# Kernel tuning notes

Hardware: AMD Instinct MI355X
Metric: run time of the kernel (lower is better)

## Reference

```python
import jax, jax.numpy as jnp
import numpy as np

DIM = 1024
NHEADS = 16
DIM_HEAD = 64
HIDDEN = NHEADS * DIM_HEAD  # 1024


def _xavier(key, fan_in, fan_out):
    limit = np.sqrt(6.0 / (fan_in + fan_out))
    return jax.random.uniform(key, (fan_in, fan_out), jnp.float32, -limit, limit)


def setup_inputs() -> dict:
    key = jax.random.key(0)
    kq, k1, k2, k3 = jax.random.split(key, 4)
    q = jax.random.normal(kq, (2, 2048, DIM), jnp.float32)
    Wq = _xavier(k1, DIM, HIDDEN)
    bq = jnp.zeros((HIDDEN,), jnp.float32)
    Wkv = _xavier(k2, DIM, 2 * HIDDEN)
    bkv = jnp.zeros((2 * HIDDEN,), jnp.float32)
    Wo = _xavier(k3, HIDDEN, DIM)
    bo = jnp.zeros((DIM,), jnp.float32)
    return {"q": q, "Wq": Wq, "bq": bq, "Wkv": Wkv, "bkv": bkv, "Wo": Wo, "bo": bo}


def reference(q, Wq, bq, Wkv, bkv, Wo, bo):
    scale = DIM_HEAD ** (-0.5)
    query = q @ Wq + bq                      # [b, s, hidden]
    kv = q @ Wkv + bkv                       # self-attention: kv from q
    key_, value = jnp.split(kv, 2, axis=-1)  # [b, s, hidden] each
    b, s, _ = query.shape
    query = query.reshape(b, s, NHEADS, DIM_HEAD)
    key_ = key_.reshape(b, s, NHEADS, DIM_HEAD)
    value = value.reshape(b, s, NHEADS, DIM_HEAD)
    scores = jnp.einsum('bqhd,bkhd->bhqk', query, key_) * scale
    attn = jax.nn.softmax(scores, axis=-1)
    out = jnp.einsum('bhqk,bkhd->bqhd', attn, value)
    out = out.reshape(b, s, HIDDEN)
    return out @ Wo + bo
```

## Files before the change

kernel.cpp:

```cpp
#include <hip/hip_runtime.h>

#define DIM 1024
#define NHEADS 16
#define DH 64
#define BATCH 2
#define SEQ 2048

typedef float f32x4 __attribute__((ext_vector_type(4)));
typedef short s16x8 __attribute__((ext_vector_type(8)));

__device__ __forceinline__ short f2bf(float f) {
    union { float f; unsigned u; } v; v.f = f;
    unsigned r = v.u + 0x7fffu + ((v.u >> 16) & 1u);
    return (short)(r >> 16);
}

__device__ __forceinline__ void gld16(const void* g, void* l) {
    __builtin_amdgcn_global_load_lds(
        (const __attribute__((address_space(1))) void*)g,
        (__attribute__((address_space(3))) void*)l, 16, 0, 0);
}

__global__ __launch_bounds__(256) void convert_bf16_kernel(
    const float* __restrict__ X, short* __restrict__ Y)
{
    const int i = (blockIdx.x * 256 + threadIdx.x) * 8;
    float4 a = *(const float4*)(X + i);
    float4 b = *(const float4*)(X + i + 4);
    s16x8 o;
    o[0] = f2bf(a.x); o[1] = f2bf(a.y); o[2] = f2bf(a.z); o[3] = f2bf(a.w);
    o[4] = f2bf(b.x); o[5] = f2bf(b.y); o[6] = f2bf(b.z); o[7] = f2bf(b.w);
    *(s16x8*)(Y + i) = o;
}

__global__ __launch_bounds__(256) void transpose_bf16_kernel(
    const float* __restrict__ W, short* __restrict__ WT, int N)
{
    const int t  = threadIdx.x;
    const int n  = blockIdx.x * 64 + (t & 63);
    const int k0 = (blockIdx.y * 4 + (t >> 6)) * 8;
    s16x8 o;
#pragma unroll
    for (int j = 0; j < 8; ++j) o[j] = f2bf(W[(size_t)(k0 + j) * N + n]);
    *(s16x8*)&WT[(size_t)n * 1024 + k0] = o;
}

template<int TM, bool OUT_BF16>
__global__ __launch_bounds__(256) void gemm_mfma_kernel(
    const short* __restrict__ A, const short* __restrict__ Bt,
    const float* __restrict__ bias, void* __restrict__ C, int M, int N)
{
    const int K = 1024;
    constexpr int NI = (TM == 128) ? 4 : 2;
    __shared__ short As[TM * 32];
    __shared__ short Bs[128 * 32];

    const int t    = threadIdx.x;
    const int wave = t >> 6;
    const int lane = t & 63;
    const int col  = lane & 15;
    const int quad = lane >> 4;
    const int m0 = blockIdx.y * TM;
    const int n0 = blockIdx.x * 128;
    const int wroff = (TM == 128) ? (wave >> 1) * 64 : 0;
    const int wcoff = (TM == 128) ? (wave & 1) * 64 : wave * 32;

    f32x4 acc[4][NI];
#pragma unroll
    for (int mi = 0; mi < 4; ++mi)
#pragma unroll
        for (int ni = 0; ni < NI; ++ni) acc[mi][ni] = (f32x4){0.f, 0.f, 0.f, 0.f};

    constexpr int RPW = TM / 4;
    const int ldrowA = wave * RPW + (lane >> 2);
    const int ldrowB = wave * 32  + (lane >> 2);
    const int ldcol  = (lane & 3) * 8;
    const short* Ag = A  + (size_t)(m0 + ldrowA) * K + ldcol;
    const short* Bg = Bt + (size_t)(n0 + ldrowB) * K + ldcol;
    short* AsW = &As[wave * RPW * 32];
    short* BsW = &Bs[wave * 1024];

    for (int k0 = 0; k0 < K; k0 += 32) {
        __syncthreads();
        gld16(Ag + k0, AsW);
        if (TM == 128) gld16(Ag + 16 * K + k0, AsW + 512);
        gld16(Bg + k0,          BsW);
        gld16(Bg + 16 * K + k0, BsW + 512);
        __syncthreads();

        s16x8 aA[4], bB[NI];
#pragma unroll
        for (int mi = 0; mi < 4; ++mi)
            aA[mi] = *(const s16x8*)&As[(wroff + 16 * mi + col) * 32 + quad * 8];
#pragma unroll
        for (int ni = 0; ni < NI; ++ni)
            bB[ni] = *(const s16x8*)&Bs[(wcoff + 16 * ni + col) * 32 + quad * 8];
#pragma unroll
        for (int mi = 0; mi < 4; ++mi)
#pragma unroll
            for (int ni = 0; ni < NI; ++ni)
                acc[mi][ni] = __builtin_amdgcn_mfma_f32_16x16x32_bf16(aA[mi], bB[ni], acc[mi][ni], 0, 0, 0);
    }

    float bias_v[NI];
#pragma unroll
    for (int ni = 0; ni < NI; ++ni) bias_v[ni] = bias[n0 + wcoff + 16 * ni + col];

#pragma unroll
    for (int mi = 0; mi < 4; ++mi)
#pragma unroll
        for (int ni = 0; ni < NI; ++ni)
#pragma unroll
            for (int r = 0; r < 4; ++r) {
                const int gm = m0 + wroff + 16 * mi + quad * 4 + r;
                const int gn = n0 + wcoff + 16 * ni + col;
                float v = acc[mi][ni][r] + bias_v[ni];
                if (OUT_BF16) ((short*)C)[(size_t)gm * N + gn] = f2bf(v);
                else          ((float*)C)[(size_t)gm * N + gn] = v;
            }
}

__global__ __launch_bounds__(256) void attn_mfma_kernel(
    const short* __restrict__ Q,
    const short* __restrict__ KV,
    short* __restrict__ O)
{
    const int qt = blockIdx.x;
    const int h  = blockIdx.y;
    const int b  = blockIdx.z;
    const int t  = threadIdx.x;
    const int wave = t >> 6;
    const int lane = t & 63;
    const int col  = lane & 15;
    const int quad = lane >> 4;

    __shared__ short Ps[128 * 72];
    __shared__ short Ks[64 * 72];
    __shared__ short Vt[64 * 72];

    const short* Qg = Q  + ((size_t)(b * SEQ + qt * 128)) * DIM + h * DH;
    const short* Kg = KV + (size_t)b * SEQ * (2 * DIM) + h * DH;
    const short* Vg = Kg + DIM;
    short*       Og = O  + ((size_t)(b * SEQ + qt * 128)) * DIM + h * DH;

    const int L_r = t >> 3;
    const int L_c = (t & 7) * 8;

#pragma unroll
    for (int p = 0; p < 4; ++p) {
        int rr = p * 32 + L_r;
        *(s16x8*)&Ps[rr * 72 + L_c] = *(const s16x8*)(Qg + (size_t)rr * DIM + L_c);
    }
    __syncthreads();

    const int qb = wave * 32;
    s16x8 aQ[2][2];
#pragma unroll
    for (int mi = 0; mi < 2; ++mi)
#pragma unroll
        for (int kq = 0; kq < 2; ++kq)
            aQ[mi][kq] = *(const s16x8*)&Ps[(qb + 16 * mi + col) * 72 + kq * 32 + quad * 8];

    f32x4 oa[2][4];
    float lsum[2][4];
#pragma unroll
    for (int mi = 0; mi < 2; ++mi) {
#pragma unroll
        for (int tt = 0; tt < 4; ++tt) oa[mi][tt] = (f32x4){0.f, 0.f, 0.f, 0.f};
#pragma unroll
        for (int r = 0; r < 4; ++r) lsum[mi][r] = 0.f;
    }

    s16x8 kx[2], vx[2];
#pragma unroll
    for (int p = 0; p < 2; ++p) {
        size_t go = (size_t)(p * 32 + L_r) * (2 * DIM) + L_c;
        kx[p] = *(const s16x8*)(Kg + go);
        vx[p] = *(const s16x8*)(Vg + go);
    }

    for (int kt = 0; kt < SEQ / 64; ++kt) {
        __syncthreads();
#pragma unroll
        for (int p = 0; p < 2; ++p) {
            int rr = p * 32 + L_r;
            *(s16x8*)&Ks[rr * 72 + L_c] = kx[p];
#pragma unroll
            for (int jj = 0; jj < 8; ++jj) {
                int dv = L_c + jj;
                Vt[dv * 72 + (rr & 7) + 8 * (((rr >> 3) ^ (dv >> 3)) & 7)] = vx[p][jj];
            }
        }
        {
            int nt = (kt + 1 < SEQ / 64) ? kt + 1 : kt;
            const short* Kt = Kg + (size_t)(nt * 64) * (2 * DIM);
            const short* Vv = Vg + (size_t)(nt * 64) * (2 * DIM);
#pragma unroll
            for (int p = 0; p < 2; ++p) {
                size_t go = (size_t)(p * 32 + L_r) * (2 * DIM) + L_c;
                kx[p] = *(const s16x8*)(Kt + go);
                vx[p] = *(const s16x8*)(Vv + go);
            }
        }
        __syncthreads();

        s16x8 bK[4][2];
#pragma unroll
        for (int tt = 0; tt < 4; ++tt)
#pragma unroll
            for (int kq = 0; kq < 2; ++kq)
                bK[tt][kq] = *(const s16x8*)&Ks[(16 * tt + col) * 72 + kq * 32 + quad * 8];
        f32x4 sc[2][4];
#pragma unroll
        for (int mi = 0; mi < 2; ++mi)
#pragma unroll
            for (int tt = 0; tt < 4; ++tt) {
                f32x4 a = (f32x4){0.f, 0.f, 0.f, 0.f};
                a = __builtin_amdgcn_mfma_f32_16x16x32_bf16(aQ[mi][0], bK[tt][0], a, 0, 0, 0);
                a = __builtin_amdgcn_mfma_f32_16x16x32_bf16(aQ[mi][1], bK[tt][1], a, 0, 0, 0);
                sc[mi][tt] = a;
            }

#pragma unroll
        for (int mi = 0; mi < 2; ++mi)
#pragma unroll
            for (int tt = 0; tt < 4; ++tt)
#pragma unroll
                for (int r = 0; r < 4; ++r) {
                    float p = __expf(sc[mi][tt][r] * 0.125f);
                    lsum[mi][r] += p;
                    Ps[(qb + 16 * mi + quad * 4 + r) * 72 + 16 * tt + col] = f2bf(p);
                }

        asm volatile("s_waitcnt lgkmcnt(0)" ::: "memory");

        s16x8 aP[2][2];
#pragma unroll
        for (int mi = 0; mi < 2; ++mi)
#pragma unroll
            for (int ks = 0; ks < 2; ++ks)
                aP[mi][ks] = *(const s16x8*)&Ps[(qb + 16 * mi + col) * 72 + ks * 32 + quad * 8];
#pragma unroll
        for (int tt = 0; tt < 4; ++tt) {
            const int dv = 16 * tt + col;
            s16x8 bv0 = *(const s16x8*)&Vt[dv * 72 + 8 * ((quad     ^ (dv >> 3)) & 7)];
            s16x8 bv1 = *(const s16x8*)&Vt[dv * 72 + 8 * (((4 + quad) ^ (dv >> 3)) & 7)];
#pragma unroll
            for (int mi = 0; mi < 2; ++mi) {
                oa[mi][tt] = __builtin_amdgcn_mfma_f32_16x16x32_bf16(aP[mi][0], bv0, oa[mi][tt], 0, 0, 0);
                oa[mi][tt] = __builtin_amdgcn_mfma_f32_16x16x32_bf16(aP[mi][1], bv1, oa[mi][tt], 0, 0, 0);
            }
        }
    }

    float inv[2][4];
#pragma unroll
    for (int mi = 0; mi < 2; ++mi)
#pragma unroll
        for (int r = 0; r < 4; ++r) {
            float s = lsum[mi][r];
            s += __shfl_xor(s, 1);
            s += __shfl_xor(s, 2);
            s += __shfl_xor(s, 4);
            s += __shfl_xor(s, 8);
            inv[mi][r] = 1.f / s;
        }
#pragma unroll
    for (int mi = 0; mi < 2; ++mi)
#pragma unroll
        for (int tt = 0; tt < 4; ++tt)
#pragma unroll
            for (int r = 0; r < 4; ++r)
                Og[(size_t)(qb + 16 * mi + quad * 4 + r) * DIM + 16 * tt + col] =
                    f2bf(oa[mi][tt][r] * inv[mi][r]);
}

extern "C" void kernel_launch(void* const* d_in, const int* in_sizes, int n_in,
                              void* d_out, int out_size, void* d_ws, size_t ws_size,
                              hipStream_t stream)
{
    const float* q   = (const float*)d_in[0];
    const float* Wq  = (const float*)d_in[1];
    const float* bq  = (const float*)d_in[2];
    const float* Wkv = (const float*)d_in[3];
    const float* bkv = (const float*)d_in[4];
    const float* Wo  = (const float*)d_in[5];
    const float* bo  = (const float*)d_in[6];
    float* out = (float*)d_out;

    const int M = BATCH * SEQ;

    short* qb    = (short*)d_ws;
    short* WqT   = qb    + (size_t)M * DIM;
    short* WkvT  = WqT   + (size_t)DIM * DIM;
    short* WoT   = WkvT  + (size_t)DIM * 2 * DIM;
    short* Qbuf  = WoT   + (size_t)DIM * DIM;
    short* KVbuf = Qbuf  + (size_t)M * DIM;
    short* AObuf = KVbuf + (size_t)M * 2 * DIM;

    convert_bf16_kernel<<<(M * DIM) / (256 * 8), 256, 0, stream>>>(q, qb);
    transpose_bf16_kernel<<<dim3(DIM / 64, 32), 256, 0, stream>>>(Wq, WqT, DIM);
    transpose_bf16_kernel<<<dim3(2 * DIM / 64, 32), 256, 0, stream>>>(Wkv, WkvT, 2 * DIM);
    transpose_bf16_kernel<<<dim3(DIM / 64, 32), 256, 0, stream>>>(Wo, WoT, DIM);

    gemm_mfma_kernel<64, true><<<dim3(DIM / 128, M / 64), 256, 0, stream>>>(qb, WqT, bq, Qbuf, M, DIM);
    gemm_mfma_kernel<128, true><<<dim3(2 * DIM / 128, M / 128), 256, 0, stream>>>(qb, WkvT, bkv, KVbuf, M, 2 * DIM);
    attn_mfma_kernel<<<dim3(SEQ / 128, NHEADS, BATCH), 256, 0, stream>>>(Qbuf, KVbuf, AObuf);
    gemm_mfma_kernel<64, false><<<dim3(DIM / 128, M / 64), 256, 0, stream>>>(AObuf, WoT, bo, out, M, DIM);
}
```

Before: 224.7 us.

## Fuse Q and KV projections and rewrite attention with split-K waves

```diff
diff --git a/kernel.cpp b/kernel.cpp
--- a/kernel.cpp
+++ b/kernel.cpp
@@ -8,6 +8,7 @@
 
 typedef float f32x4 __attribute__((ext_vector_type(4)));
 typedef short s16x8 __attribute__((ext_vector_type(8)));
+typedef short s16x4 __attribute__((ext_vector_type(4)));
 
 __device__ __forceinline__ short f2bf(float f) {
     union { float f; unsigned u; } v; v.f = f;
@@ -48,7 +49,8 @@
 template<int TM, bool OUT_BF16>
 __global__ __launch_bounds__(256) void gemm_mfma_kernel(
     const short* __restrict__ A, const short* __restrict__ Bt,
-    const float* __restrict__ bias, void* __restrict__ C, int M, int N)
+    const float* __restrict__ bias0, const float* __restrict__ bias1, int nsplit,
+    void* __restrict__ C, int M, int N)
 {
     const int K = 1024;
     constexpr int NI = (TM == 128) ? 4 : 2;
@@ -104,7 +106,10 @@
 
     float bias_v[NI];
 #pragma unroll
-    for (int ni = 0; ni < NI; ++ni) bias_v[ni] = bias[n0 + wcoff + 16 * ni + col];
+    for (int ni = 0; ni < NI; ++ni) {
+        int nb = n0 + wcoff + 16 * ni + col;
+        bias_v[ni] = (nb < nsplit) ? bias0[nb] : bias1[nb - nsplit];
+    }
 
 #pragma unroll
     for (int mi = 0; mi < 4; ++mi)
@@ -120,9 +125,8 @@
             }
 }
 
-__global__ __launch_bounds__(256) void attn_mfma_kernel(
-    const short* __restrict__ Q,
-    const short* __restrict__ KV,
+__global__ __launch_bounds__(512) void attn_v5_kernel(
+    const short* __restrict__ QKV,
     short* __restrict__ O)
 {
     const int qt = blockIdx.x;
@@ -133,146 +137,158 @@
     const int lane = t & 63;
     const int col  = lane & 15;
     const int quad = lane >> 4;
-
-    __shared__ short Ps[128 * 72];
-    __shared__ short Ks[64 * 72];
-    __shared__ short Vt[64 * 72];
-
-    const short* Qg = Q  + ((size_t)(b * SEQ + qt * 128)) * DIM + h * DH;
-    const short* Kg = KV + (size_t)b * SEQ * (2 * DIM) + h * DH;
-    const short* Vg = Kg + DIM;
-    short*       Og = O  + ((size_t)(b * SEQ + qt * 128)) * DIM + h * DH;
-
-    const int L_r = t >> 3;
-    const int L_c = (t & 7) * 8;
-
-#pragma unroll
-    for (int p = 0; p < 4; ++p) {
-        int rr = p * 32 + L_r;
-        *(s16x8*)&Ps[rr * 72 + L_c] = *(const s16x8*)(Qg + (size_t)rr * DIM + L_c);
-    }
-    __syncthreads();
-
-    const int qb = wave * 32;
-    s16x8 aQ[2][2];
-#pragma unroll
-    for (int mi = 0; mi < 2; ++mi)
+    const int wq = wave & 3;
+    const int kh = wave >> 2;
+
+    __shared__ short Ks[2][64 * 72];
+    __shared__ short Vt[2][64 * 72];
+    __shared__ short Ps[8][64 * 40];
+
+    const short* Qg = QKV + (size_t)(b * SEQ + qt * 256) * 3072 + h * DH;
+    const short* Kg = QKV + (size_t)(b * SEQ) * 3072 + 1024 + h * DH;
+    const short* Vg = Kg + 1024;
+
+    s16x8 aQ[4][2];
+#pragma unroll
+    for (int tq = 0; tq < 4; ++tq)
 #pragma unroll
         for (int kq = 0; kq < 2; ++kq)
-            aQ[mi][kq] = *(const s16x8*)&Ps[(qb + 16 * mi + col) * 72 + kq * 32 + quad * 8];
-
-    f32x4 oa[2][4];
-    float lsum[2][4];
-#pragma unroll
-    for (int mi = 0; mi < 2; ++mi) {
-#pragma unroll
-        for (int tt = 0; tt < 4; ++tt) oa[mi][tt] = (f32x4){0.f, 0.f, 0.f, 0.f};
-#pragma unroll
-        for (int r = 0; r < 4; ++r) lsum[mi][r] = 0.f;
-    }
-
-    s16x8 kx[2], vx[2];
-#pragma unroll
-    for (int p = 0; p < 2; ++p) {
-        size_t go = (size_t)(p * 32 + L_r) * (2 * DIM) + L_c;
-        kx[p] = *(const s16x8*)(Kg + go);
-        vx[p] = *(const s16x8*)(Vg + go);
-    }
+            aQ[tq][kq] = *(const s16x8*)(Qg + (size_t)(wq * 64 + 16 * tq + col) * 3072 + kq * 32 + quad * 8);
+
+    f32x4 oa[4][4];
+    float lsum[4] = {0.f, 0.f, 0.f, 0.f};
+#pragma unroll
+    for (int td = 0; td < 4; ++td)
+#pragma unroll
+        for (int tq = 0; tq < 4; ++tq) oa[td][tq] = (f32x4){0.f, 0.f, 0.f, 0.f};
+
+    const int srow = t >> 3;
+    const int sc8  = (t & 7) * 8;
+    const short* KgS = Kg + (size_t)srow * 3072 + sc8;
+    const short* VgS = Vg + (size_t)srow * 3072 + sc8;
+    s16x8 kx = *(const s16x8*)KgS;
+    s16x8 vx = *(const s16x8*)VgS;
+
+    short* PsW = &Ps[wave][0];
 
     for (int kt = 0; kt < SEQ / 64; ++kt) {
-        __syncthreads();
-#pragma unroll
-        for (int p = 0; p < 2; ++p) {
-            int rr = p * 32 + L_r;
-            *(s16x8*)&Ks[rr * 72 + L_c] = kx[p];
-#pragma unroll
-            for (int jj = 0; jj < 8; ++jj) {
-                int dv = L_c + jj;
-                Vt[dv * 72 + (rr & 7) + 8 * (((rr >> 3) ^ (dv >> 3)) & 7)] = vx[p][jj];
-            }
+        const int cur = kt & 1;
+        *(s16x8*)&Ks[cur][srow * 72 + sc8] = kx;
+#pragma unroll
+        for (int jj = 0; jj < 8; ++jj) {
+            int dv = sc8 + jj;
+            Vt[cur][dv * 72 + (srow & 7) + 8 * (((srow >> 3) ^ (dv >> 3)) & 7)] = vx[jj];
         }
         {
             int nt = (kt + 1 < SEQ / 64) ? kt + 1 : kt;
-            const short* Kt = Kg + (size_t)(nt * 64) * (2 * DIM);
-            const short* Vv = Vg + (size_t)(nt * 64) * (2 * DIM);
-#pragma unroll
-            for (int p = 0; p < 2; ++p) {
-                size_t go = (size_t)(p * 32 + L_r) * (2 * DIM) + L_c;
-                kx[p] = *(const s16x8*)(Kt + go);
-                vx[p] = *(const s16x8*)(Vv + go);
+            kx = *(const s16x8*)(KgS + (size_t)nt * 64 * 3072);
+            vx = *(const s16x8*)(VgS + (size_t)nt * 64 * 3072);
+        }
+        __syncthreads();
+
+        s16x8 aK[2][2];
+#pragma unroll
+        for (int tk = 0; tk < 2; ++tk)
+#pragma unroll
+            for (int kq = 0; kq < 2; ++kq)
+                aK[tk][kq] = *(const s16x8*)&Ks[cur][(kh * 32 + 16 * tk + col) * 72 + kq * 32 + quad * 8];
+        f32x4 st[2][4];
+#pragma unroll
+        for (int tk = 0; tk < 2; ++tk)
+#pragma unroll
+            for (int tq = 0; tq < 4; ++tq) {
+                f32x4 a = (f32x4){0.f, 0.f, 0.f, 0.f};
+                a = __builtin_amdgcn_mfma_f32_16x16x32_bf16(aK[tk][0], aQ[tq][0], a, 0, 0, 0);
+                a = __builtin_amdgcn_mfma_f32_16x16x32_bf16(aK[tk][1], aQ[tq][1], a, 0, 0, 0);
+                st[tk][tq] = a;
             }
-        }
-        __syncthreads();
-
-        s16x8 bK[4][2];
-#pragma unroll
-        for (int tt = 0; tt < 4; ++tt)
-#pragma unroll
-            for (int kq = 0; kq < 2; ++kq)
-                bK[tt][kq] = *(const s16x8*)&Ks[(16 * tt + col) * 72 + kq * 32 + quad * 8];
-        f32x4 sc[2][4];
-#pragma unroll
-        for (int mi = 0; mi < 2; ++mi)
-#pragma unroll
-            for (int tt = 0; tt < 4; ++tt) {
-                f32x4 a = (f32x4){0.f, 0.f, 0.f, 0.f};
-                a = __builtin_amdgcn_mfma_f32_16x16x32_bf16(aQ[mi][0], bK[tt][0], a, 0, 0, 0);
-                a = __builtin_amdgcn_mfma_f32_16x16x32_bf16(aQ[mi][1], bK[tt][1], a, 0, 0, 0);
-                sc[mi][tt] = a;
+
+#pragma unroll
+        for (int tk = 0; tk < 2; ++tk)
+#pragma unroll
+            for (int tq = 0; tq < 4; ++tq) {
+                float p0 = __expf(st[tk][tq][0] * 0.125f);
+                float p1 = __expf(st[tk][tq][1] * 0.125f);
+                float p2 = __expf(st[tk][tq][2] * 0.125f);
+                float p3 = __expf(st[tk][tq][3] * 0.125f);
+                lsum[tq] += (p0 + p1) + (p2 + p3);
+                s16x4 pk;
+                pk[0] = f2bf(p0); pk[1] = f2bf(p1); pk[2] = f2bf(p2); pk[3] = f2bf(p3);
+                *(s16x4*)&PsW[(16 * tq + col) * 40 + 16 * tk + quad * 4] = pk;
             }
-
-#pragma unroll
-        for (int mi = 0; mi < 2; ++mi)
-#pragma unroll
-            for (int tt = 0; tt < 4; ++tt)
-#pragma unroll
-                for (int r = 0; r < 4; ++r) {
-                    float p = __expf(sc[mi][tt][r] * 0.125f);
-                    lsum[mi][r] += p;
-                    Ps[(qb + 16 * mi + quad * 4 + r) * 72 + 16 * tt + col] = f2bf(p);
-                }
-
         asm volatile("s_waitcnt lgkmcnt(0)" ::: "memory");
 
-        s16x8 aP[2][2];
-#pragma unroll
-        for (int mi = 0; mi < 2; ++mi)
-#pragma unroll
-            for (int ks = 0; ks < 2; ++ks)
-                aP[mi][ks] = *(const s16x8*)&Ps[(qb + 16 * mi + col) * 72 + ks * 32 + quad * 8];
-#pragma unroll
-        for (int tt = 0; tt < 4; ++tt) {
-            const int dv = 16 * tt + col;
-            s16x8 bv0 = *(const s16x8*)&Vt[dv * 72 + 8 * ((quad     ^ (dv >> 3)) & 7)];
-            s16x8 bv1 = *(const s16x8*)&Vt[dv * 72 + 8 * (((4 + quad) ^ (dv >> 3)) & 7)];
-#pragma unroll
-            for (int mi = 0; mi < 2; ++mi) {
-                oa[mi][tt] = __builtin_amdgcn_mfma_f32_16x16x32_bf16(aP[mi][0], bv0, oa[mi][tt], 0, 0, 0);
-                oa[mi][tt] = __builtin_amdgcn_mfma_f32_16x16x32_bf16(aP[mi][1], bv1, oa[mi][tt], 0, 0, 0);
+        s16x8 bP[4];
+#pragma unroll
+        for (int tq = 0; tq < 4; ++tq)
+            bP[tq] = *(const s16x8*)&PsW[(16 * tq + col) * 40 + quad * 8];
+#pragma unroll
+        for (int td = 0; td < 4; ++td) {
+            const int dv = 16 * td + col;
+            s16x8 aV = *(const s16x8*)&Vt[cur][dv * 72 + 8 * (((kh * 4 + quad) ^ (dv >> 3)) & 7)];
+#pragma unroll
+            for (int tq = 0; tq < 4; ++tq)
+                oa[td][tq] = __builtin_amdgcn_mfma_f32_16x16x32_bf16(aV, bP[tq], oa[td][tq], 0, 0, 0);
+        }
+    }
+
+#pragma unroll
+    for (int tq = 0; tq < 4; ++tq) {
+        lsum[tq] += __shfl_xor(lsum[tq], 16);
+        lsum[tq] += __shfl_xor(lsum[tq], 32);
+    }
+
+    __syncthreads();
+    float* red  = (float*)&Ps[0][0];
+    float* redl = red + 8192;
+#pragma unroll
+    for (int round = 0; round < 2; ++round) {
+        if (wave >= 4 && ((wave >> 1) & 1) == round) {
+            const int slot = wave & 1;
+#pragma unroll
+            for (int td = 0; td < 4; ++td)
+#pragma unroll
+                for (int tq = 0; tq < 4; ++tq)
+#pragma unroll
+                    for (int r = 0; r < 4; ++r)
+                        red[slot * 4096 + (16 * td + quad * 4 + r) * 64 + 16 * tq + col] = oa[td][tq][r];
+            if (quad == 0)
+#pragma unroll
+                for (int tq = 0; tq < 4; ++tq)
+                    redl[slot * 64 + 16 * tq + col] = lsum[tq];
+        }
+        __syncthreads();
+        if (wave < 4 && ((wave >> 1) & 1) == round) {
+            const int slot = wave & 1;
+#pragma unroll
+            for (int td = 0; td < 4; ++td)
+#pragma unroll
+                for (int tq = 0; tq < 4; ++tq)
+#pragma unroll
+                    for (int r = 0; r < 4; ++r)
+                        oa[td][tq][r] += red[slot * 4096 + (16 * td + quad * 4 + r) * 64 + 16 * tq + col];
+#pragma unroll
+            for (int tq = 0; tq < 4; ++tq)
+                lsum[tq] += redl[slot * 64 + 16 * tq + col];
+        }
+        __syncthreads();
+    }
+
+    if (wave < 4) {
+        short* Og = O + (size_t)(b * SEQ + qt * 256 + wq * 64) * DIM + h * DH;
+        float inv[4];
+#pragma unroll
+        for (int tq = 0; tq < 4; ++tq) inv[tq] = 1.f / lsum[tq];
+#pragma unroll
+        for (int td = 0; td < 4; ++td)
+#pragma unroll
+            for (int tq = 0; tq < 4; ++tq) {
+                s16x4 v;
+#pragma unroll
+                for (int r = 0; r < 4; ++r) v[r] = f2bf(oa[td][tq][r] * inv[tq]);
+                *(s16x4*)(Og + (size_t)(16 * tq + col) * DIM + 16 * td + quad * 4) = v;
             }
-        }
-    }
-
-    float inv[2][4];
-#pragma unroll
-    for (int mi = 0; mi < 2; ++mi)
-#pragma unroll
-        for (int r = 0; r < 4; ++r) {
-            float s = lsum[mi][r];
-            s += __shfl_xor(s, 1);
-            s += __shfl_xor(s, 2);
-            s += __shfl_xor(s, 4);
-            s += __shfl_xor(s, 8);
-            inv[mi][r] = 1.f / s;
-        }
-#pragma unroll
-    for (int mi = 0; mi < 2; ++mi)
-#pragma unroll
-        for (int tt = 0; tt < 4; ++tt)
-#pragma unroll
-            for (int r = 0; r < 4; ++r)
-                Og[(size_t)(qb + 16 * mi + quad * 4 + r) * DIM + 16 * tt + col] =
-                    f2bf(oa[mi][tt][r] * inv[mi][r]);
+    }
 }
 
 extern "C" void kernel_launch(void* const* d_in, const int* in_sizes, int n_in,
@@ -290,21 +306,20 @@
 
     const int M = BATCH * SEQ;
 
-    short* qb    = (short*)d_ws;
-    short* WqT   = qb    + (size_t)M * DIM;
-    short* WkvT  = WqT   + (size_t)DIM * DIM;
-    short* WoT   = WkvT  + (size_t)DIM * 2 * DIM;
-    short* Qbuf  = WoT   + (size_t)DIM * DIM;
-    short* KVbuf = Qbuf  + (size_t)M * DIM;
-    short* AObuf = KVbuf + (size_t)M * 2 * DIM;
+    short* qb     = (short*)d_ws;
+    short* WqkvT  = qb     + (size_t)M * DIM;
+    short* WoT    = WqkvT  + (size_t)3 * DIM * DIM;
+    short* QKVbuf = WoT    + (size_t)DIM * DIM;
+    short* AObuf  = QKVbuf + (size_t)M * 3 * DIM;
 
     convert_bf16_kernel<<<(M * DIM) / (256 * 8), 256, 0, stream>>>(q, qb);
-    transpose_bf16_kernel<<<dim3(DIM / 64, 32), 256, 0, stream>>>(Wq, WqT, DIM);
-    transpose_bf16_kernel<<<dim3(2 * DIM / 64, 32), 256, 0, stream>>>(Wkv, WkvT, 2 * DIM);
+    transpose_bf16_kernel<<<dim3(DIM / 64, 32), 256, 0, stream>>>(Wq, WqkvT, DIM);
+    transpose_bf16_kernel<<<dim3(2 * DIM / 64, 32), 256, 0, stream>>>(Wkv, WqkvT + (size_t)DIM * DIM, 2 * DIM);
     transpose_bf16_kernel<<<dim3(DIM / 64, 32), 256, 0, stream>>>(Wo, WoT, DIM);
 
-    gemm_mfma_kernel<64, true><<<dim3(DIM / 128, M / 64), 256, 0, stream>>>(qb, WqT, bq, Qbuf, M, DIM);
-    gemm_mfma_kernel<128, true><<<dim3(2 * DIM / 128, M / 128), 256, 0, stream>>>(qb, WkvT, bkv, KVbuf, M, 2 * DIM);
-    attn_mfma_kernel<<<dim3(SEQ / 128, NHEADS, BATCH), 256, 0, stream>>>(Qbuf, KVbuf, AObuf);
-    gemm_mfma_kernel<64, false><<<dim3(DIM / 128, M / 64), 256, 0, stream>>>(AObuf, WoT, bo, out, M, DIM);
-}
+    gemm_mfma_kernel<128, true><<<dim3(3 * DIM / 128, M / 128), 256, 0, stream>>>(
+        qb, WqkvT, bq, bkv, DIM, QKVbuf, M, 3 * DIM);
+    attn_v5_kernel<<<dim3(SEQ / 256, NHEADS, BATCH), 512, 0, stream>>>(QKVbuf, AObuf);
+    gemm_mfma_kernel<64, false><<<dim3(DIM / 128, M / 64), 256, 0, stream>>>(
+        AObuf, WoT, bo, bo, 1 << 30, out, M, DIM);
+}
```

Result: faster. 202.6 us (-9.8%).
